# Kernel tuning notes

Hardware: AMD Instinct MI355X
Metric: run time of the kernel (lower is better)

The kernel has to match this reference:

```python
import jax, jax.numpy as jnp
import numpy as np

DIM = 768; DEPTH = 12; D_STATE = 64; D_CONV = 4; EXPAND = 2; HEADDIM = 64
VOCAB = 2048; MAXSEQ = 4096; B = 4; L = 2048
D_INNER = EXPAND * DIM            # 1536
NHEADS = D_INNER // HEADDIM       # 24
NG = 1                            # ngroups (Mamba2 default)
CONV_DIM = D_INNER + 2 * NG * D_STATE
D_IN_PROJ = 2 * D_INNER + 2 * NG * D_STATE + NHEADS
EPS = 1e-5


def silu(x):
    return x * jax.nn.sigmoid(x)


def layernorm(x, w, b):
    m = jnp.mean(x, -1, keepdims=True)
    v = jnp.mean((x - m) ** 2, -1, keepdims=True)
    return (x - m) * jax.lax.rsqrt(v + EPS) * w + b


def mamba2(x, in_w, cw, cb, dtb, a_log, dh, nw, ow):
    # x: (b, l, DIM)
    b, l, _ = x.shape
    zxbcdt = x @ in_w.T  # (b, l, D_IN_PROJ)
    z, xBC, dt = jnp.split(zxbcdt, [D_INNER, D_INNER + CONV_DIM], axis=-1)
    # causal depthwise conv1d over time
    xBC_p = jnp.pad(xBC, ((0, 0), (D_CONV - 1, 0), (0, 0))).transpose(0, 2, 1)  # (b, c, l+pad)
    conv = jax.lax.conv_general_dilated(
        xBC_p, cw[:, None, :], (1,), 'VALID',
        feature_group_count=CONV_DIM, dimension_numbers=('NCH', 'OIH', 'NCH'))
    xBC = silu(conv.transpose(0, 2, 1) + cb)  # (b, l, CONV_DIM)
    xs, Bm, Cm = jnp.split(xBC, [D_INNER, D_INNER + NG * D_STATE], axis=-1)
    xs = xs.reshape(b, l, NHEADS, HEADDIM)                # (b,l,h,p)
    dt = jax.nn.softplus(dt + dtb)                        # (b,l,h)
    A = -jnp.exp(a_log)                                   # (h,)
    dA = jnp.exp(dt * A)                                  # (b,l,h) decay per step

    def step(h, inp):
        # h: (b,h,p,n) SSM state
        dA_t, dt_t, x_t, B_t, C_t = inp
        dBx = jnp.einsum('bh,bhp,bn->bhpn', dt_t, x_t, B_t)
        h = h * dA_t[..., None, None] + dBx
        y = jnp.einsum('bhpn,bn->bhp', h, C_t)
        return h, y

    h0 = jnp.zeros((b, NHEADS, HEADDIM, D_STATE), x.dtype)
    xsT = (dA.transpose(1, 0, 2), dt.transpose(1, 0, 2), xs.transpose(1, 0, 2, 3),
           Bm.transpose(1, 0, 2), Cm.transpose(1, 0, 2))
    _, ys = jax.lax.scan(step, h0, xsT)                   # (l,b,h,p)
    y = ys.transpose(1, 0, 2, 3) + dh[None, None, :, None] * xs
    y = y.reshape(b, l, D_INNER)
    # gated RMSNorm (norm of y*silu(z)), then output projection
    y = y * silu(z)
    y = y * jax.lax.rsqrt(jnp.mean(y * y, -1, keepdims=True) + EPS) * nw
    return y @ ow.T


def setup_inputs() -> dict:
    key = jax.random.key(0)
    ks = jax.random.split(key, 12)
    init = lambda k, shape, s=0.02: (jax.random.normal(k, shape) * s).astype(jnp.float32)
    inp = {
        'token_emb': init(ks[0], (VOCAB, DIM)),
        'pos_emb': init(ks[1], (MAXSEQ, DIM)),
        'ln_w': jnp.ones((DEPTH, DIM), jnp.float32),
        'ln_b': jnp.zeros((DEPTH, DIM), jnp.float32),
        'in_proj_w': init(ks[2], (DEPTH, D_IN_PROJ, DIM)),
        'conv_w': init(ks[3], (DEPTH, CONV_DIM, D_CONV), 0.2),
        'conv_b': jnp.zeros((DEPTH, CONV_DIM), jnp.float32),
        'dt_bias': init(ks[4], (DEPTH, NHEADS), 0.5),
        'A_log': jnp.log(jax.random.uniform(ks[5], (DEPTH, NHEADS), minval=1.0, maxval=16.0)).astype(jnp.float32),
        'D_param': jnp.ones((DEPTH, NHEADS), jnp.float32),
        'norm_w': jnp.ones((DEPTH, D_INNER), jnp.float32),
        'out_proj_w': init(ks[6], (DEPTH, DIM, D_INNER)),
        'normf_w': jnp.ones((DIM,), jnp.float32),
        'normf_b': jnp.zeros((DIM,), jnp.float32),
        'head_w': init(ks[7], (VOCAB, DIM)),
        'input_ids': jax.random.randint(ks[8], (B, L), 0, VOCAB),
        'labels': jax.random.randint(ks[9], (B, L), 0, VOCAB),
    }
    return inp


def reference(token_emb, pos_emb, ln_w, ln_b, in_proj_w, conv_w, conv_b, dt_bias,
              A_log, D_param, norm_w, out_proj_w, normf_w, normf_b, head_w,
              input_ids, labels):
    b, n = input_ids.shape
    positions = jnp.arange(n) % MAXSEQ
    x = token_emb[input_ids] + pos_emb[positions][None]   # (b, n, DIM)

    def layer_fn(xc, p):
        lw, lb, iw, cw, cb, dtb, alog, dh, nw, ow = p
        return xc + mamba2(layernorm(xc, lw, lb), iw, cw, cb, dtb, alog, dh, nw, ow), None

    x, _ = jax.lax.scan(layer_fn, x,
                        (ln_w, ln_b, in_proj_w, conv_w, conv_b, dt_bias,
                         A_log, D_param, norm_w, out_proj_w))
    x = layernorm(x, normf_w, normf_b)
    logits = x @ head_w.T                                  # (b, n, VOCAB)
    sl = logits[:, :-1, :].reshape(-1, VOCAB)
    tl = labels[:, 1:].reshape(-1)
    logp = jax.nn.log_softmax(sl, -1)
    loss = -jnp.take_along_axis(logp, tl[:, None], axis=1).mean()
    return loss, logits
```

## Files before the change

### kernel.cpp

```cpp
#include <hip/hip_runtime.h>
#include <hip/hip_bf16.h>
#include <stdint.h>

#define DIMM   768
#define NLAYER 12
#define DST    64
#define DINNER 1536
#define NH     24
#define CONVD  1664
#define DINP   3224
#define NB     4
#define LL     2048
#define ROWS   (NB*LL)
#define VOC    2048
#define Q      128
#define NCH    (LL/Q)

typedef float f32x4 __attribute__((ext_vector_type(4)));
typedef short s16x8 __attribute__((ext_vector_type(8)));

#define MFMA(acc, a, b) asm volatile("v_mfma_f32_16x16x32_bf16 %0, %1, %2, %0" : "+v"(acc) : "v"(a), "v"(b))
#define FENCE4(v) asm volatile("s_nop 7" : "+v"(v))
#define GLL16(g, l) __builtin_amdgcn_global_load_lds( \
    (const __attribute__((address_space(1))) uint32_t*)(g), \
    (__attribute__((address_space(3))) uint32_t*)(l), 16, 0, 0)

__device__ __forceinline__ unsigned short f2bf(float f) {
  unsigned int u = __float_as_uint(f);
  u = (u + 0x7fffu + ((u >> 16) & 1u)) >> 16;
  return (unsigned short)u;
}
__device__ __forceinline__ float bf2f(unsigned short u) {
  return __uint_as_float(((unsigned int)u) << 16);
}
__device__ __forceinline__ float softplus_f(float v) {
  return (v > 20.f) ? v : log1pf(__expf(v));
}

__device__ __forceinline__ uint4 pack8(float4 a, float4 b) {
  union { unsigned short us[8]; uint4 q; } pk;
  pk.us[0] = f2bf(a.x); pk.us[1] = f2bf(a.y); pk.us[2] = f2bf(a.z); pk.us[3] = f2bf(a.w);
  pk.us[4] = f2bf(b.x); pk.us[5] = f2bf(b.y); pk.us[6] = f2bf(b.z); pk.us[7] = f2bf(b.w);
  return pk.q;
}

__device__ __forceinline__ float blk_sum(float v, float* red, int tid) {
  #pragma unroll
  for (int o = 32; o > 0; o >>= 1) v += __shfl_down(v, o, 64);
  __syncthreads();
  if ((tid & 63) == 0) red[tid >> 6] = v;
  __syncthreads();
  return red[0] + red[1] + red[2] + red[3];
}

__device__ __forceinline__ float blk_max(float v, float* red, int tid) {
  #pragma unroll
  for (int o = 32; o > 0; o >>= 1) v = fmaxf(v, __shfl_down(v, o, 64));
  __syncthreads();
  if ((tid & 63) == 0) red[tid >> 6] = v;
  __syncthreads();
  return fmaxf(fmaxf(red[0], red[1]), fmaxf(red[2], red[3]));
}

__global__ __launch_bounds__(256) void cvt_kernel(
    const float* __restrict__ s, unsigned short* __restrict__ d, int n8)
{
  int i = blockIdx.x * 256 + threadIdx.x;
  if (i < n8) {
    float4 a = ((const float4*)s)[i*2];
    float4 b = ((const float4*)s)[i*2 + 1];
    ((uint4*)d)[i] = pack8(a, b);
  }
}

__global__ __launch_bounds__(256) void cvtlayer_kernel(
    const float* __restrict__ ip, const float* __restrict__ op,
    const float* __restrict__ nw, unsigned short* __restrict__ ipb,
    unsigned short* __restrict__ opb)
{
  const int ipn8 = DINP*DIMM/8;
  const int opn8 = DIMM*DINNER/8;
  int i = blockIdx.x * 256 + threadIdx.x;
  if (i < ipn8) {
    float4 a = ((const float4*)ip)[i*2];
    float4 b = ((const float4*)ip)[i*2 + 1];
    ((uint4*)ipb)[i] = pack8(a, b);
  } else if (i < ipn8 + opn8) {
    int j = i - ipn8;
    int k = (j*8) % DINNER;
    float4 a = ((const float4*)op)[j*2];
    float4 b = ((const float4*)op)[j*2 + 1];
    float4 na = *(const float4*)(nw + k);
    float4 nb = *(const float4*)(nw + k + 4);
    a.x *= na.x; a.y *= na.y; a.z *= na.z; a.w *= na.w;
    b.x *= nb.x; b.y *= nb.y; b.z *= nb.z; b.w *= nb.w;
    ((uint4*)opb)[j] = pack8(a, b);
  }
}

__global__ __launch_bounds__(256) void embed_kernel(
    const float* __restrict__ tok, const float* __restrict__ pos,
    const int* __restrict__ ids, float* __restrict__ X)
{
  int idx = blockIdx.x * 256 + threadIdx.x;
  int row = idx / DIMM, d = idx % DIMM;
  int l = row & (LL - 1);
  X[idx] = tok[(size_t)ids[row] * DIMM + d] + pos[(size_t)l * DIMM + d];
}

__global__ __launch_bounds__(256) void ln_kernel(
    const float* __restrict__ X, const float* __restrict__ w,
    const float* __restrict__ b, unsigned short* __restrict__ Ob)
{
  __shared__ float red[8];
  int row = blockIdx.x, tid = threadIdx.x;
  const float* x = X + (size_t)row * DIMM;
  float v0 = x[tid], v1 = x[tid + 256], v2 = x[tid + 512];
  float mean = blk_sum(v0 + v1 + v2, red, tid) * (1.f / 768.f);
  float d0 = v0 - mean, d1 = v1 - mean, d2 = v2 - mean;
  float var = blk_sum(d0*d0 + d1*d1 + d2*d2, red, tid) * (1.f / 768.f);
  float rs = rsqrtf(var + 1e-5f);
  unsigned short* ob = Ob + (size_t)row * DIMM;
  ob[tid]       = f2bf(d0 * rs * w[tid]       + b[tid]);
  ob[tid + 256] = f2bf(d1 * rs * w[tid + 256] + b[tid + 256]);
  ob[tid + 512] = f2bf(d2 * rs * w[tid + 512] + b[tid + 512]);
}

template<int OUTM>
__global__ __launch_bounds__(256) void gemm_kernel(
    const unsigned short* __restrict__ A, const unsigned short* __restrict__ W,
    void* __restrict__ Cp, const float* __restrict__ RS,
    int Nreal, int K, int lda, int ldw, int ldc)
{
  __shared__ unsigned short As[128*32];
  __shared__ unsigned short Bs[128*32];
  const int tid = threadIdx.x;
  const int wave = tid >> 6, lane = tid & 63;
  const int wr = wave >> 1, wc = wave & 1;
  const int l15 = lane & 15, l4 = lane >> 4;
  const int bm = blockIdx.x * 128, bn = blockIdx.y * 128;
  f32x4 acc[4][4] = {};

  const int srow = lane >> 2;
  const int scol = (lane & 3) * 8;
  const unsigned short* aptr[2];
  const unsigned short* wptr[2];
  unsigned short* alds[2];
  unsigned short* blds[2];
  #pragma unroll
  for (int j = 0; j < 2; j++) {
    int row = (wave*2 + j)*16 + srow;
    aptr[j] = A + (size_t)(bm + row) * lda + scol;
    int wrow = bn + row; if (wrow > Nreal - 1) wrow = Nreal - 1;
    wptr[j] = W + (size_t)wrow * ldw + scol;
    alds[j] = &As[(wave*2 + j) * 512];
    blds[j] = &Bs[(wave*2 + j) * 512];
  }

  for (int k0 = 0; k0 < K; k0 += 32) {
    __syncthreads();
    #pragma unroll
    for (int j = 0; j < 2; j++) {
      GLL16(aptr[j], alds[j]);
      GLL16(wptr[j], blds[j]);
      aptr[j] += 32; wptr[j] += 32;
    }
    __syncthreads();
    s16x8 af[4], bfr[4];
    #pragma unroll
    for (int mi = 0; mi < 4; mi++)
      af[mi] = *(const s16x8*)&As[(wr*64 + mi*16 + l15)*32 + l4*8];
    #pragma unroll
    for (int ni = 0; ni < 4; ni++)
      bfr[ni] = *(const s16x8*)&Bs[(wc*64 + ni*16 + l15)*32 + l4*8];
    #pragma unroll
    for (int mi = 0; mi < 4; mi++)
      #pragma unroll
      for (int ni = 0; ni < 4; ni++)
        MFMA(acc[mi][ni], af[mi], bfr[ni]);
  }
  #pragma unroll
  for (int mi = 0; mi < 4; mi++)
    #pragma unroll
    for (int ni = 0; ni < 4; ni++)
      FENCE4(acc[mi][ni]);
  const int row0 = bm + wr*64 + l4*4;
  const int colb = bn + wc*64 + l15;
  #pragma unroll
  for (int mi = 0; mi < 4; mi++) {
    #pragma unroll
    for (int ni = 0; ni < 4; ni++) {
      int col = colb + ni*16;
      if (col < Nreal) {
        #pragma unroll
        for (int r = 0; r < 4; r++) {
          int rowm = row0 + mi*16 + r;
          size_t idx = (size_t)rowm * ldc + col;
          if (OUTM == 0)      ((float*)Cp)[idx] = acc[mi][ni][r];
          else if (OUTM == 1) ((float*)Cp)[idx] += RS[rowm] * acc[mi][ni][r];
          else                ((unsigned short*)Cp)[idx] = f2bf(acc[mi][ni][r]);
        }
      }
    }
  }
}

__global__ __launch_bounds__(256) void conv_kernel(
    const unsigned short* __restrict__ ZX, const float* __restrict__ cw,
    const float* __restrict__ cb, unsigned short* __restrict__ XC)
{
  int idx = blockIdx.x * 256 + threadIdx.x;
  int c8 = idx % 208, row = idx / 208;
  int c = c8 * 8;
  int l = row & (LL - 1);
  const unsigned short* z = ZX + (size_t)row * DINP + DINNER + c;
  s16x8 x0 = *(const s16x8*)z;
  s16x8 x1 = {}, x2 = {}, x3 = {};
  bool h1 = l >= 1, h2 = l >= 2, h3 = l >= 3;
  if (h1) x1 = *(const s16x8*)(z - DINP);
  if (h2) x2 = *(const s16x8*)(z - 2*DINP);
  if (h3) x3 = *(const s16x8*)(z - 3*DINP);
  union { unsigned short us[8]; uint4 q; } o;
  #pragma unroll
  for (int j = 0; j < 8; j++) {
    float4 w = ((const float4*)cw)[c + j];
    float a = cb[c + j] + bf2f((unsigned short)x0[j]) * w.w;
    if (h1) a += bf2f((unsigned short)x1[j]) * w.z;
    if (h2) a += bf2f((unsigned short)x2[j]) * w.y;
    if (h3) a += bf2f((unsigned short)x3[j]) * w.x;
    o.us[j] = f2bf(a / (1.f + __expf(-a)));
  }
  *(uint4*)(XC + (size_t)row * CONVD + c) = o.q;
}

__global__ __launch_bounds__(256) void chunkstate_kernel(
    const unsigned short* __restrict__ XC_, const unsigned short* __restrict__ ZX_,
    const float* __restrict__ dtbp, const float* __restrict__ alogp,
    float* __restrict__ HC_)
{
  __shared__ unsigned short XT[64*136];
  __shared__ unsigned short BT[64*136];
  __shared__ float cum_sh[Q], wgt_sh[Q];
  __shared__ float carry;
  const int tid = threadIdx.x;
  const int b = blockIdx.x >> 4, c = blockIdx.x & 15, h = blockIdx.y;
  const size_t row0 = (size_t)b*LL + c*Q;

  const float dtbv = dtbp[h];
  const float nA = -__expf(alogp[h]);
  float v = 0.f, dtv = 0.f;
  if (tid < Q) {
    float vraw = bf2f(ZX_[(row0 + tid)*DINP + 3200 + h]) + dtbv;
    dtv = softplus_f(vraw);
    v = dtv * nA;
    #pragma unroll
    for (int off = 1; off < 64; off <<= 1) {
      float u = __shfl_up(v, off, 64);
      if ((tid & 63) >= off) v += u;
    }
  }
  if (tid == 63) carry = v;
  __syncthreads();
  if (tid >= 64 && tid < Q) v += carry;
  if (tid < Q) cum_sh[tid] = v;
  __syncthreads();
  if (tid < Q) wgt_sh[tid] = __expf(cum_sh[Q-1] - v) * dtv;
  __syncthreads();

  const int p  = tid & 63;
  const int s0 = (tid >> 6) * 2;
  const unsigned short* xb = XC_ + row0 * CONVD;
  #pragma unroll
  for (int i = 0; i < 16; i++) {
    int s = s0 + i*8;
    float x0 = bf2f(xb[(size_t)s*CONVD     + h*64 + p]) * wgt_sh[s];
    float x1 = bf2f(xb[(size_t)(s+1)*CONVD + h*64 + p]) * wgt_sh[s+1];
    *(unsigned int*)&XT[p*136 + s] = (unsigned int)f2bf(x0) | ((unsigned int)f2bf(x1) << 16);
    unsigned int bb = (unsigned int)xb[(size_t)s*CONVD + DINNER + p]
                    | ((unsigned int)xb[(size_t)(s+1)*CONVD + DINNER + p] << 16);
    *(unsigned int*)&BT[p*136 + s] = bb;
  }
  __syncthreads();

  const int wave = tid >> 6, lane = tid & 63, l15 = lane & 15, l4 = lane >> 4;
  const int wr = wave >> 1, wc = wave & 1;
  f32x4 acc[2][2] = {};
  #pragma unroll
  for (int ks = 0; ks < 4; ks++) {
    int kof = ks*32 + l4*8;
    s16x8 a0 = *(const s16x8*)&XT[(wr*32      + l15)*136 + kof];
    s16x8 a1 = *(const s16x8*)&XT[(wr*32 + 16 + l15)*136 + kof];
    s16x8 b0 = *(const s16x8*)&BT[(wc*32      + l15)*136 + kof];
    s16x8 b1 = *(const s16x8*)&BT[(wc*32 + 16 + l15)*136 + kof];
    MFMA(acc[0][0], a0, b0); MFMA(acc[0][1], a0, b1);
    MFMA(acc[1][0], a1, b0); MFMA(acc[1][1], a1, b1);
  }
  #pragma unroll
  for (int mi = 0; mi < 2; mi++)
    #pragma unroll
    for (int ni = 0; ni < 2; ni++)
      FENCE4(acc[mi][ni]);
  size_t base = (((size_t)(b*NH + h))*NCH + c)*4096;
  #pragma unroll
  for (int mi = 0; mi < 2; mi++)
    #pragma unroll
    for (int ni = 0; ni < 2; ni++)
      #pragma unroll
      for (int r = 0; r < 4; r++)
        HC_[base + (size_t)(wr*32 + mi*16 + l4*4 + r)*64 + wc*32 + ni*16 + l15] = acc[mi][ni][r];
}

__global__ __launch_bounds__(256) void scan2_kernel(
    const float* __restrict__ HC_, float* __restrict__ HIN_,
    const unsigned short* __restrict__ ZX_, const float* __restrict__ dtbp,
    const float* __restrict__ alogp)
{
  __shared__ float dec[NCH];
  int bh = blockIdx.x, b = bh / NH, h = bh % NH;
  int q = blockIdx.y;
  int t = threadIdx.x;
  const float dtbv = dtbp[h];
  const float nA = -__expf(alogp[h]);
  float part = 0.f;
  #pragma unroll
  for (int i = 0; i < 8; i++) {
    float vraw = bf2f(ZX_[((size_t)b*LL + t*8 + i)*DINP + 3200 + h]) + dtbv;
    part += softplus_f(vraw) * nA;
  }
  #pragma unroll
  for (int off = 1; off < 16; off <<= 1) part += __shfl_xor(part, off, 16);
  if ((t & 15) == 0) dec[t >> 4] = __expf(part);
  __syncthreads();
  float st[4] = {0.f, 0.f, 0.f, 0.f};
  for (int c = 0; c < NCH; c++) {
    float d = dec[c];
    size_t base = ((size_t)bh*NCH + c)*4096 + q*1024;
    #pragma unroll
    for (int i = 0; i < 4; i++) {
      int idx = i*256 + t;
      HIN_[base + idx] = st[i];
      st[i] = st[i]*d + HC_[base + idx];
    }
  }
}

__global__ __launch_bounds__(256) void ydec_kernel(
    const unsigned short* __restrict__ XC_, const unsigned short* __restrict__ ZX_,
    const float* __restrict__ dtbp, const float* __restrict__ alogp,
    const float* __restrict__ HIN_, const float* __restrict__ Dp_,
    unsigned short* __restrict__ Y_)
{
  __shared__ unsigned short POOL[128*72*2];
  __shared__ unsigned short Hs[64*72];
  __shared__ unsigned short XTs[64*136];
  __shared__ float cum_sh[Q], dt_sh[Q];
  __shared__ float carry;
  unsigned short* Cs = POOL;
  unsigned short* Bs = POOL + 128*72;
  unsigned short* Ms = POOL;

  const int tid = threadIdx.x;
  const int b = blockIdx.x >> 4, c = blockIdx.x & 15, h = blockIdx.y;
  const size_t row0 = (size_t)b*LL + c*Q;

  const float dtbv = dtbp[h];
  const float nA = -__expf(alogp[h]);
  float v = 0.f, dtv = 0.f;
  if (tid < Q) {
    float vraw = bf2f(ZX_[(row0 + tid)*DINP + 3200 + h]) + dtbv;
    dtv = softplus_f(vraw);
    v = dtv * nA;
    #pragma unroll
    for (int off = 1; off < 64; off <<= 1) {
      float u = __shfl_up(v, off, 64);
      if ((tid & 63) >= off) v += u;
    }
  }
  if (tid == 63) carry = v;
  __syncthreads();
  if (tid >= 64 && tid < Q) v += carry;
  if (tid < Q) { cum_sh[tid] = v; dt_sh[tid] = dtv; }

  const int p  = tid & 63;
  const int s0 = (tid >> 6) * 2;
  const unsigned short* xb = XC_ + row0 * CONVD;
  #pragma unroll
  for (int i = 0; i < 16; i++) {
    int s = s0 + i*8;
    Cs[(size_t)s*72 + p]     = xb[(size_t)s*CONVD     + DINNER + DST + p];
    Cs[(size_t)(s+1)*72 + p] = xb[(size_t)(s+1)*CONVD + DINNER + DST + p];
    Bs[(size_t)s*72 + p]     = xb[(size_t)s*CONVD     + DINNER + p];
    Bs[(size_t)(s+1)*72 + p] = xb[(size_t)(s+1)*CONVD + DINNER + p];
    unsigned int xx = (unsigned int)xb[(size_t)s*CONVD + h*64 + p]
                    | ((unsigned int)xb[(size_t)(s+1)*CONVD + h*64 + p] << 16);
    *(unsigned int*)&XTs[p*136 + s] = xx;
  }
  {
    size_t hb = (((size_t)(b*NH + h))*NCH + c)*4096;
    #pragma unroll
    for (int i = 0; i < 16; i++) {
      int idx = i*256 + tid;
      Hs[(idx >> 6)*72 + (idx & 63)] = f2bf(HIN_[hb + idx]);
    }
  }
  __syncthreads();

  const int wv = tid >> 6, lane = tid & 63, l15 = lane & 15, l4 = lane >> 4;
  const int tb = wv * 32;

  f32x4 g[2][8] = {};
  f32x4 yacc[2][4] = {};
  #pragma unroll
  for (int ks = 0; ks < 2; ks++) {
    int kof = ks*32 + l4*8;
    s16x8 a0 = *(const s16x8*)&Cs[(size_t)(tb      + l15)*72 + kof];
    s16x8 a1 = *(const s16x8*)&Cs[(size_t)(tb + 16 + l15)*72 + kof];
    #pragma unroll
    for (int ni = 0; ni < 8; ni++) {
      if (ni <= 2*wv + 1) {
        s16x8 bfr = *(const s16x8*)&Bs[(size_t)(ni*16 + l15)*72 + kof];
        if (ni <= 2*wv) MFMA(g[0][ni], a0, bfr);
        MFMA(g[1][ni], a1, bfr);
      }
    }
    #pragma unroll
    for (int ni2 = 0; ni2 < 4; ni2++) {
      s16x8 hf = *(const s16x8*)&Hs[(size_t)(ni2*16 + l15)*72 + kof];
      MFMA(yacc[0][ni2], a0, hf);
      MFMA(yacc[1][ni2], a1, hf);
    }
  }
  __syncthreads();

  #pragma unroll
  for (int mi = 0; mi < 2; mi++) {
    #pragma unroll
    for (int ni = 0; ni < 8; ni++) {
      FENCE4(g[mi][ni]);
      int t0 = tb + mi*16 + l4*4;
      int s  = ni*16 + l15;
      float ds = dt_sh[s], cs = cum_sh[s];
      #pragma unroll
      for (int r = 0; r < 4; r++) {
        int tt = t0 + r;
        float val = (s <= tt) ? g[mi][ni][r] * __expf(cum_sh[tt] - cs) * ds : 0.f;
        Ms[(size_t)tt*136 + s] = f2bf(val);
      }
    }
  }

  float er[2][4];
  #pragma unroll
  for (int mi = 0; mi < 2; mi++)
    #pragma unroll
    for (int r = 0; r < 4; r++)
      er[mi][r] = __expf(cum_sh[tb + mi*16 + l4*4 + r]);
  #pragma unroll
  for (int mi = 0; mi < 2; mi++)
    #pragma unroll
    for (int ni2 = 0; ni2 < 4; ni2++) {
      FENCE4(yacc[mi][ni2]);
      #pragma unroll
      for (int r = 0; r < 4; r++) yacc[mi][ni2][r] *= er[mi][r];
      FENCE4(yacc[mi][ni2]);
    }

  #pragma unroll
  for (int ks = 0; ks < 4; ks++) {
    int kof = ks*32 + l4*8;
    s16x8 a0 = *(const s16x8*)&Ms[(size_t)(tb      + l15)*136 + kof];
    s16x8 a1 = *(const s16x8*)&Ms[(size_t)(tb + 16 + l15)*136 + kof];
    #pragma unroll
    for (int ni2 = 0; ni2 < 4; ni2++) {
      s16x8 xf = *(const s16x8*)&XTs[(size_t)(ni2*16 + l15)*136 + kof];
      MFMA(yacc[0][ni2], a0, xf);
      MFMA(yacc[1][ni2], a1, xf);
    }
  }
  #pragma unroll
  for (int mi = 0; mi < 2; mi++)
    #pragma unroll
    for (int ni2 = 0; ni2 < 4; ni2++)
      FENCE4(yacc[mi][ni2]);

  float Dv = Dp_[h];
  #pragma unroll
  for (int mi = 0; mi < 2; mi++) {
    #pragma unroll
    for (int ni2 = 0; ni2 < 4; ni2++) {
      #pragma unroll
      for (int r = 0; r < 4; r++) {
        int t = tb + mi*16 + l4*4 + r;
        int pc = ni2*16 + l15;
        float xv = bf2f(XTs[pc*136 + t]);
        float yv = yacc[mi][ni2][r] + Dv * xv;
        size_t row = row0 + t;
        float zv = bf2f(ZX_[row*DINP + h*64 + pc]);
        Y_[row*DINNER + h*64 + pc] = f2bf(yv * (zv / (1.f + __expf(-zv))));
      }
    }
  }
}

__global__ __launch_bounds__(256) void rs_kernel(
    const unsigned short* __restrict__ Y, float* __restrict__ RS)
{
  __shared__ float red[8];
  int row = blockIdx.x, tid = threadIdx.x;
  const unsigned short* y = Y + (size_t)row * DINNER;
  float sq = 0.f;
  if (tid < 192) {
    s16x8 u = *(const s16x8*)&y[tid*8];
    #pragma unroll
    for (int i = 0; i < 8; i++) { float f = bf2f((unsigned short)u[i]); sq += f*f; }
  }
  float ms = blk_sum(sq, red, tid) * (1.f / 1536.f);
  if (tid == 0) RS[row] = rsqrtf(ms + 1e-5f);
}

__global__ void zero_kernel(float* __restrict__ a) { a[0] = 0.f; }

__global__ __launch_bounds__(256) void loss_kernel(
    const float* __restrict__ logits, const int* __restrict__ labels,
    float* __restrict__ acc)
{
  __shared__ float red[8];
  int i = blockIdx.x;
  int b = i / (LL - 1), l = i % (LL - 1);
  const float* lr = logits + ((size_t)b * LL + l) * VOC;
  int tid = threadIdx.x;
  float4 v0 = ((const float4*)lr)[tid*2];
  float4 v1 = ((const float4*)lr)[tid*2 + 1];
  float mx = fmaxf(fmaxf(fmaxf(v0.x, v0.y), fmaxf(v0.z, v0.w)),
                   fmaxf(fmaxf(v1.x, v1.y), fmaxf(v1.z, v1.w)));
  mx = blk_max(mx, red, tid);
  float se = __expf(v0.x - mx) + __expf(v0.y - mx) + __expf(v0.z - mx) + __expf(v0.w - mx)
           + __expf(v1.x - mx) + __expf(v1.y - mx) + __expf(v1.z - mx) + __expf(v1.w - mx);
  se = blk_sum(se, red, tid);
  if (tid == 0) {
    int lab = labels[b * LL + l + 1];
    float lp = lr[lab] - mx - __logf(se);
    atomicAdd(acc, -lp);
  }
}

__global__ void fin_kernel(float* __restrict__ out, const float* __restrict__ acc) {
  out[0] = acc[0] * (1.f / 8188.f);
}

extern "C" void kernel_launch(void* const* d_in, const int* in_sizes, int n_in,
                              void* d_out, int out_size, void* d_ws, size_t ws_size,
                              hipStream_t stream)
{
  const float* tok  = (const float*)d_in[0];
  const float* pos  = (const float*)d_in[1];
  const float* lnw  = (const float*)d_in[2];
  const float* lnb  = (const float*)d_in[3];
  const float* ipw  = (const float*)d_in[4];
  const float* cw   = (const float*)d_in[5];
  const float* cb   = (const float*)d_in[6];
  const float* dtb  = (const float*)d_in[7];
  const float* alog = (const float*)d_in[8];
  const float* dpar = (const float*)d_in[9];
  const float* nw   = (const float*)d_in[10];
  const float* opw  = (const float*)d_in[11];
  const float* nfw  = (const float*)d_in[12];
  const float* nfb  = (const float*)d_in[13];
  const float* hw   = (const float*)d_in[14];
  const int*   ids  = (const int*)d_in[15];
  const int*   labs = (const int*)d_in[16];
  float* out = (float*)d_out;

  char* ws = (char*)d_ws;
  float*          X    = (float*)(ws);
  unsigned short* ZX   = (unsigned short*)(ws +  25165824ull);
  unsigned short* XC   = (unsigned short*)(ws +  77987840ull);
  unsigned short* Ybf  = (unsigned short*)(ws + 105250816ull);
  unsigned short* XNb  = (unsigned short*)(ws + 130416640ull);
  unsigned short* IPWb = (unsigned short*)(ws + 142999552ull);
  unsigned short* OPWb = (unsigned short*)(ws + 147951616ull);
  unsigned short* HWb  = (unsigned short*)(ws + 150310912ull);
  float*          HC   = (float*)(ws + 153456640ull);
  float*          RS   = (float*)(ws + 178622464ull);
  float*          ACC  = (float*)(ws + 178655232ull);
  float*          HIN  = out + 1 + 8388608;

  embed_kernel<<<ROWS*DIMM/256, 256, 0, stream>>>(tok, pos, ids, X);
  cvt_kernel<<<(VOC*DIMM/8 + 255)/256, 256, 0, stream>>>(hw, HWb, VOC*DIMM/8);

  const int cvtg = (DINP*DIMM/8 + DIMM*DINNER/8 + 255)/256;
  for (int l = 0; l < NLAYER; l++) {
    cvtlayer_kernel<<<cvtg, 256, 0, stream>>>(
        ipw + (size_t)l*DINP*DIMM, opw + (size_t)l*DIMM*DINNER,
        nw + (size_t)l*DINNER, IPWb, OPWb);

    ln_kernel<<<ROWS, 256, 0, stream>>>(X, lnw + l*DIMM, lnb + l*DIMM, XNb);

    dim3 g1(64, 26);
    gemm_kernel<2><<<g1, 256, 0, stream>>>(XNb, IPWb, ZX, nullptr,
                                           DINP, DIMM, DIMM, DIMM, DINP);

    conv_kernel<<<ROWS*208/256, 256, 0, stream>>>(ZX, cw + l*CONVD*4, cb + l*CONVD, XC);

    dim3 gs(NB*NCH, NH);
    chunkstate_kernel<<<gs, 256, 0, stream>>>(XC, ZX, dtb + l*NH, alog + l*NH, HC);
    dim3 g2s(NB*NH, 4);
    scan2_kernel<<<g2s, 256, 0, stream>>>(HC, HIN, ZX, dtb + l*NH, alog + l*NH);
    ydec_kernel<<<gs, 256, 0, stream>>>(XC, ZX, dtb + l*NH, alog + l*NH, HIN,
                                        dpar + l*NH, Ybf);

    rs_kernel<<<ROWS, 256, 0, stream>>>(Ybf, RS);

    dim3 g2(64, 6);
    gemm_kernel<1><<<g2, 256, 0, stream>>>(Ybf, OPWb, X, RS,
                                           DIMM, DINNER, DINNER, DINNER, DIMM);
  }

  ln_kernel<<<ROWS, 256, 0, stream>>>(X, nfw, nfb, XNb);
  dim3 g3(64, 16);
  gemm_kernel<0><<<g3, 256, 0, stream>>>(XNb, HWb, out + 1, nullptr,
                                         VOC, DIMM, DIMM, DIMM, VOC);

  zero_kernel<<<1, 1, 0, stream>>>(ACC);
  loss_kernel<<<NB*(LL-1), 256, 0, stream>>>(out + 1, labs, ACC);
  fin_kernel<<<1, 1, 0, stream>>>(out, ACC);
}
```

Measured before the change: 3.105 ms.

## Batch weight conversion, fuse RMS norm into ydec, cache dt cumsums, wave-per-row loss

All layer weights are now converted to bf16 in a single launch up front instead of once per layer. The sum-of-squares for the gated RMSNorm is accumulated in ydec via atomics, which removes rs_kernel. The chunkstate kernel stores the per-step dt cumsums and chunk decays so that scan2 and ydec no longer recompute softplus and prefix sums. The loss kernel uses one wave per row. The trade-offs are extra workspace, atomic float adds with nondeterministic summation order, and scratch buffers placed inside the output region.

```diff
diff --git a/kernel.cpp b/kernel.cpp
--- a/kernel.cpp
+++ b/kernel.cpp
@@ -53,48 +53,35 @@
   return red[0] + red[1] + red[2] + red[3];
 }
 
-__device__ __forceinline__ float blk_max(float v, float* red, int tid) {
-  #pragma unroll
-  for (int o = 32; o > 0; o >>= 1) v = fmaxf(v, __shfl_down(v, o, 64));
-  __syncthreads();
-  if ((tid & 63) == 0) red[tid >> 6] = v;
-  __syncthreads();
-  return fmaxf(fmaxf(red[0], red[1]), fmaxf(red[2], red[3]));
-}
-
-__global__ __launch_bounds__(256) void cvt_kernel(
-    const float* __restrict__ s, unsigned short* __restrict__ d, int n8)
-{
+__global__ __launch_bounds__(256) void cvtall_kernel(
+    const float* __restrict__ ipw, const float* __restrict__ opw,
+    const float* __restrict__ nw, const float* __restrict__ hw,
+    unsigned short* __restrict__ ipb, unsigned short* __restrict__ opb,
+    unsigned short* __restrict__ hwb)
+{
+  const int IPN8 = NLAYER*DINP*DIMM/8;
+  const int OPN8 = NLAYER*DIMM*DINNER/8;
+  const int HWN8 = VOC*DIMM/8;
   int i = blockIdx.x * 256 + threadIdx.x;
-  if (i < n8) {
-    float4 a = ((const float4*)s)[i*2];
-    float4 b = ((const float4*)s)[i*2 + 1];
-    ((uint4*)d)[i] = pack8(a, b);
-  }
-}
-
-__global__ __launch_bounds__(256) void cvtlayer_kernel(
-    const float* __restrict__ ip, const float* __restrict__ op,
-    const float* __restrict__ nw, unsigned short* __restrict__ ipb,
-    unsigned short* __restrict__ opb)
-{
-  const int ipn8 = DINP*DIMM/8;
-  const int opn8 = DIMM*DINNER/8;
-  int i = blockIdx.x * 256 + threadIdx.x;
-  if (i < ipn8) {
-    float4 a = ((const float4*)ip)[i*2];
-    float4 b = ((const float4*)ip)[i*2 + 1];
+  if (i < IPN8) {
+    float4 a = ((const float4*)ipw)[i*2];
+    float4 b = ((const float4*)ipw)[i*2 + 1];
     ((uint4*)ipb)[i] = pack8(a, b);
-  } else if (i < ipn8 + opn8) {
-    int j = i - ipn8;
+  } else if (i < IPN8 + OPN8) {
+    int j = i - IPN8;
+    int layer = j / (DIMM*DINNER/8);
     int k = (j*8) % DINNER;
-    float4 a = ((const float4*)op)[j*2];
-    float4 b = ((const float4*)op)[j*2 + 1];
-    float4 na = *(const float4*)(nw + k);
-    float4 nb = *(const float4*)(nw + k + 4);
+    const float* nwl = nw + layer*DINNER;
+    float4 a = ((const float4*)opw)[j*2];
+    float4 b = ((const float4*)opw)[j*2 + 1];
+    float4 na = *(const float4*)(nwl + k);
+    float4 nb = *(const float4*)(nwl + k + 4);
     a.x *= na.x; a.y *= na.y; a.z *= na.z; a.w *= na.w;
     b.x *= nb.x; b.y *= nb.y; b.z *= nb.z; b.w *= nb.w;
     ((uint4*)opb)[j] = pack8(a, b);
+  } else if (i < IPN8 + OPN8 + HWN8) {
+    int j = i - IPN8 - OPN8;
+    ((uint4*)hwb)[j] = pack8(((const float4*)hw)[j*2], ((const float4*)hw)[j*2 + 1]);
   }
 }
 
@@ -197,7 +184,10 @@
           int rowm = row0 + mi*16 + r;
           size_t idx = (size_t)rowm * ldc + col;
           if (OUTM == 0)      ((float*)Cp)[idx] = acc[mi][ni][r];
-          else if (OUTM == 1) ((float*)Cp)[idx] += RS[rowm] * acc[mi][ni][r];
+          else if (OUTM == 1) {
+            float rsv = rsqrtf(RS[rowm] * (1.f/1536.f) + 1e-5f);
+            ((float*)Cp)[idx] += rsv * acc[mi][ni][r];
+          }
           else                ((unsigned short*)Cp)[idx] = f2bf(acc[mi][ni][r]);
         }
       }
@@ -207,9 +197,11 @@
 
 __global__ __launch_bounds__(256) void conv_kernel(
     const unsigned short* __restrict__ ZX, const float* __restrict__ cw,
-    const float* __restrict__ cb, unsigned short* __restrict__ XC)
+    const float* __restrict__ cb, unsigned short* __restrict__ XC,
+    float* __restrict__ RS)
 {
   int idx = blockIdx.x * 256 + threadIdx.x;
+  if (idx < ROWS) RS[idx] = 0.f;
   int c8 = idx % 208, row = idx / 208;
   int c = c8 * 8;
   int l = row & (LL - 1);
@@ -236,7 +228,7 @@
 __global__ __launch_bounds__(256) void chunkstate_kernel(
     const unsigned short* __restrict__ XC_, const unsigned short* __restrict__ ZX_,
     const float* __restrict__ dtbp, const float* __restrict__ alogp,
-    float* __restrict__ HC_)
+    float* __restrict__ HC_, float2* __restrict__ DTC_, float* __restrict__ CDEC_)
 {
   __shared__ unsigned short XT[64*136];
   __shared__ unsigned short BT[64*136];
@@ -245,6 +237,7 @@
   const int tid = threadIdx.x;
   const int b = blockIdx.x >> 4, c = blockIdx.x & 15, h = blockIdx.y;
   const size_t row0 = (size_t)b*LL + c*Q;
+  const size_t bhc = (size_t)(b*NH + h)*NCH + c;
 
   const float dtbv = dtbp[h];
   const float nA = -__expf(alogp[h]);
@@ -264,7 +257,12 @@
   if (tid >= 64 && tid < Q) v += carry;
   if (tid < Q) cum_sh[tid] = v;
   __syncthreads();
-  if (tid < Q) wgt_sh[tid] = __expf(cum_sh[Q-1] - v) * dtv;
+  if (tid < Q) {
+    wgt_sh[tid] = __expf(cum_sh[Q-1] - v) * dtv;
+    float2 cd; cd.x = v; cd.y = dtv;
+    DTC_[bhc*Q + tid] = cd;
+  }
+  if (tid == Q-1) CDEC_[bhc] = __expf(v);
   __syncthreads();
 
   const int p  = tid & 63;
@@ -300,7 +298,7 @@
     #pragma unroll
     for (int ni = 0; ni < 2; ni++)
       FENCE4(acc[mi][ni]);
-  size_t base = (((size_t)(b*NH + h))*NCH + c)*4096;
+  size_t base = bhc*4096;
   #pragma unroll
   for (int mi = 0; mi < 2; mi++)
     #pragma unroll
@@ -312,24 +310,13 @@
 
 __global__ __launch_bounds__(256) void scan2_kernel(
     const float* __restrict__ HC_, float* __restrict__ HIN_,
-    const unsigned short* __restrict__ ZX_, const float* __restrict__ dtbp,
-    const float* __restrict__ alogp)
+    const float* __restrict__ CDEC_)
 {
   __shared__ float dec[NCH];
-  int bh = blockIdx.x, b = bh / NH, h = bh % NH;
+  int bh = blockIdx.x;
   int q = blockIdx.y;
   int t = threadIdx.x;
-  const float dtbv = dtbp[h];
-  const float nA = -__expf(alogp[h]);
-  float part = 0.f;
-  #pragma unroll
-  for (int i = 0; i < 8; i++) {
-    float vraw = bf2f(ZX_[((size_t)b*LL + t*8 + i)*DINP + 3200 + h]) + dtbv;
-    part += softplus_f(vraw) * nA;
-  }
-  #pragma unroll
-  for (int off = 1; off < 16; off <<= 1) part += __shfl_xor(part, off, 16);
-  if ((t & 15) == 0) dec[t >> 4] = __expf(part);
+  if (t < NCH) dec[t] = CDEC_[bh*NCH + t];
   __syncthreads();
   float st[4] = {0.f, 0.f, 0.f, 0.f};
   for (int c = 0; c < NCH; c++) {
@@ -346,15 +333,14 @@
 
 __global__ __launch_bounds__(256) void ydec_kernel(
     const unsigned short* __restrict__ XC_, const unsigned short* __restrict__ ZX_,
-    const float* __restrict__ dtbp, const float* __restrict__ alogp,
-    const float* __restrict__ HIN_, const float* __restrict__ Dp_,
-    unsigned short* __restrict__ Y_)
+    const float2* __restrict__ DTC_, const float* __restrict__ HIN_,
+    const float* __restrict__ Dp_, unsigned short* __restrict__ Y_,
+    float* __restrict__ RS_)
 {
   __shared__ unsigned short POOL[128*72*2];
   __shared__ unsigned short Hs[64*72];
   __shared__ unsigned short XTs[64*136];
   __shared__ float cum_sh[Q], dt_sh[Q];
-  __shared__ float carry;
   unsigned short* Cs = POOL;
   unsigned short* Bs = POOL + 128*72;
   unsigned short* Ms = POOL;
@@ -362,24 +348,12 @@
   const int tid = threadIdx.x;
   const int b = blockIdx.x >> 4, c = blockIdx.x & 15, h = blockIdx.y;
   const size_t row0 = (size_t)b*LL + c*Q;
-
-  const float dtbv = dtbp[h];
-  const float nA = -__expf(alogp[h]);
-  float v = 0.f, dtv = 0.f;
+  const size_t bhc = (size_t)(b*NH + h)*NCH + c;
+
   if (tid < Q) {
-    float vraw = bf2f(ZX_[(row0 + tid)*DINP + 3200 + h]) + dtbv;
-    dtv = softplus_f(vraw);
-    v = dtv * nA;
-    #pragma unroll
-    for (int off = 1; off < 64; off <<= 1) {
-      float u = __shfl_up(v, off, 64);
-      if ((tid & 63) >= off) v += u;
-    }
-  }
-  if (tid == 63) carry = v;
-  __syncthreads();
-  if (tid >= 64 && tid < Q) v += carry;
-  if (tid < Q) { cum_sh[tid] = v; dt_sh[tid] = dtv; }
+    float2 cd = DTC_[bhc*Q + tid];
+    cum_sh[tid] = cd.x; dt_sh[tid] = cd.y;
+  }
 
   const int p  = tid & 63;
   const int s0 = (tid >> 6) * 2;
@@ -396,7 +370,7 @@
     *(unsigned int*)&XTs[p*136 + s] = xx;
   }
   {
-    size_t hb = (((size_t)(b*NH + h))*NCH + c)*4096;
+    size_t hb = bhc*4096;
     #pragma unroll
     for (int i = 0; i < 16; i++) {
       int idx = i*256 + tid;
@@ -484,6 +458,7 @@
       FENCE4(yacc[mi][ni2]);
 
   float Dv = Dp_[h];
+  float sq[2][4] = {};
   #pragma unroll
   for (int mi = 0; mi < 2; mi++) {
     #pragma unroll
@@ -496,26 +471,23 @@
         float yv = yacc[mi][ni2][r] + Dv * xv;
         size_t row = row0 + t;
         float zv = bf2f(ZX_[row*DINP + h*64 + pc]);
-        Y_[row*DINNER + h*64 + pc] = f2bf(yv * (zv / (1.f + __expf(-zv))));
+        float yg = yv * (zv / (1.f + __expf(-zv)));
+        Y_[row*DINNER + h*64 + pc] = f2bf(yg);
+        sq[mi][r] += yg * yg;
       }
     }
   }
-}
-
-__global__ __launch_bounds__(256) void rs_kernel(
-    const unsigned short* __restrict__ Y, float* __restrict__ RS)
-{
-  __shared__ float red[8];
-  int row = blockIdx.x, tid = threadIdx.x;
-  const unsigned short* y = Y + (size_t)row * DINNER;
-  float sq = 0.f;
-  if (tid < 192) {
-    s16x8 u = *(const s16x8*)&y[tid*8];
-    #pragma unroll
-    for (int i = 0; i < 8; i++) { float f = bf2f((unsigned short)u[i]); sq += f*f; }
-  }
-  float ms = blk_sum(sq, red, tid) * (1.f / 1536.f);
-  if (tid == 0) RS[row] = rsqrtf(ms + 1e-5f);
+  #pragma unroll
+  for (int mi = 0; mi < 2; mi++) {
+    #pragma unroll
+    for (int r = 0; r < 4; r++) {
+      float vsum = sq[mi][r];
+      #pragma unroll
+      for (int off = 1; off < 16; off <<= 1) vsum += __shfl_xor(vsum, off, 64);
+      if (l15 == 0)
+        atomicAdd(&RS_[row0 + tb + mi*16 + l4*4 + r], vsum);
+    }
+  }
 }
 
 __global__ void zero_kernel(float* __restrict__ a) { a[0] = 0.f; }
@@ -524,24 +496,35 @@
     const float* __restrict__ logits, const int* __restrict__ labels,
     float* __restrict__ acc)
 {
-  __shared__ float red[8];
-  int i = blockIdx.x;
+  __shared__ float red[4];
+  int wv = threadIdx.x >> 6, lane = threadIdx.x & 63;
+  int i = blockIdx.x * 4 + wv;
   int b = i / (LL - 1), l = i % (LL - 1);
   const float* lr = logits + ((size_t)b * LL + l) * VOC;
-  int tid = threadIdx.x;
-  float4 v0 = ((const float4*)lr)[tid*2];
-  float4 v1 = ((const float4*)lr)[tid*2 + 1];
-  float mx = fmaxf(fmaxf(fmaxf(v0.x, v0.y), fmaxf(v0.z, v0.w)),
-                   fmaxf(fmaxf(v1.x, v1.y), fmaxf(v1.z, v1.w)));
-  mx = blk_max(mx, red, tid);
-  float se = __expf(v0.x - mx) + __expf(v0.y - mx) + __expf(v0.z - mx) + __expf(v0.w - mx)
-           + __expf(v1.x - mx) + __expf(v1.y - mx) + __expf(v1.z - mx) + __expf(v1.w - mx);
-  se = blk_sum(se, red, tid);
-  if (tid == 0) {
+  const float4* lr4 = (const float4*)lr;
+  float4 v[8];
+  #pragma unroll
+  for (int j = 0; j < 8; j++) v[j] = lr4[j*64 + lane];
+  float mx = -1e30f;
+  #pragma unroll
+  for (int j = 0; j < 8; j++)
+    mx = fmaxf(mx, fmaxf(fmaxf(v[j].x, v[j].y), fmaxf(v[j].z, v[j].w)));
+  #pragma unroll
+  for (int o = 32; o > 0; o >>= 1) mx = fmaxf(mx, __shfl_xor(mx, o, 64));
+  float se = 0.f;
+  #pragma unroll
+  for (int j = 0; j < 8; j++)
+    se += __expf(v[j].x - mx) + __expf(v[j].y - mx)
+        + __expf(v[j].z - mx) + __expf(v[j].w - mx);
+  #pragma unroll
+  for (int o = 32; o > 0; o >>= 1) se += __shfl_xor(se, o, 64);
+  if (lane == 0) {
     int lab = labels[b * LL + l + 1];
-    float lp = lr[lab] - mx - __logf(se);
-    atomicAdd(acc, -lp);
-  }
+    red[wv] = lr[lab] - mx - __logf(se);
+  }
+  __syncthreads();
+  if (threadIdx.x == 0)
+    atomicAdd(acc, -(red[0] + red[1] + red[2] + red[3]));
 }
 
 __global__ void fin_kernel(float* __restrict__ out, const float* __restrict__ acc) {
@@ -578,41 +561,38 @@
   unsigned short* Ybf  = (unsigned short*)(ws + 105250816ull);
   unsigned short* XNb  = (unsigned short*)(ws + 130416640ull);
   unsigned short* IPWb = (unsigned short*)(ws + 142999552ull);
-  unsigned short* OPWb = (unsigned short*)(ws + 147951616ull);
-  unsigned short* HWb  = (unsigned short*)(ws + 150310912ull);
-  float*          HC   = (float*)(ws + 153456640ull);
-  float*          RS   = (float*)(ws + 178622464ull);
-  float*          ACC  = (float*)(ws + 178655232ull);
-  float*          HIN  = out + 1 + 8388608;
+  unsigned short* OPWb = (unsigned short*)(ws + 202424320ull);
+  unsigned short* HWb  = (unsigned short*)(ws + 230735872ull);
+  float2*         DTC  = (float2*)(ws + 233881600ull);
+  float*          CDEC = (float*)(ws + 235454464ull);
+  float*          RS   = (float*)(ws + 235460608ull);
+  float*          ACC  = (float*)(ws + 235493376ull);
+  float*          HC   = out + 1;
+  float*          HIN  = out + 1 + 6291456;
 
   embed_kernel<<<ROWS*DIMM/256, 256, 0, stream>>>(tok, pos, ids, X);
-  cvt_kernel<<<(VOC*DIMM/8 + 255)/256, 256, 0, stream>>>(hw, HWb, VOC*DIMM/8);
-
-  const int cvtg = (DINP*DIMM/8 + DIMM*DINNER/8 + 255)/256;
+  {
+    const int tot = NLAYER*DINP*DIMM/8 + NLAYER*DIMM*DINNER/8 + VOC*DIMM/8;
+    cvtall_kernel<<<(tot + 255)/256, 256, 0, stream>>>(ipw, opw, nw, hw, IPWb, OPWb, HWb);
+  }
+
   for (int l = 0; l < NLAYER; l++) {
-    cvtlayer_kernel<<<cvtg, 256, 0, stream>>>(
-        ipw + (size_t)l*DINP*DIMM, opw + (size_t)l*DIMM*DINNER,
-        nw + (size_t)l*DINNER, IPWb, OPWb);
-
     ln_kernel<<<ROWS, 256, 0, stream>>>(X, lnw + l*DIMM, lnb + l*DIMM, XNb);
 
     dim3 g1(64, 26);
-    gemm_kernel<2><<<g1, 256, 0, stream>>>(XNb, IPWb, ZX, nullptr,
+    gemm_kernel<2><<<g1, 256, 0, stream>>>(XNb, IPWb + (size_t)l*DINP*DIMM, ZX, nullptr,
                                            DINP, DIMM, DIMM, DIMM, DINP);
 
-    conv_kernel<<<ROWS*208/256, 256, 0, stream>>>(ZX, cw + l*CONVD*4, cb + l*CONVD, XC);
+    conv_kernel<<<ROWS*208/256, 256, 0, stream>>>(ZX, cw + l*CONVD*4, cb + l*CONVD, XC, RS);
 
     dim3 gs(NB*NCH, NH);
-    chunkstate_kernel<<<gs, 256, 0, stream>>>(XC, ZX, dtb + l*NH, alog + l*NH, HC);
+    chunkstate_kernel<<<gs, 256, 0, stream>>>(XC, ZX, dtb + l*NH, alog + l*NH, HC, DTC, CDEC);
     dim3 g2s(NB*NH, 4);
-    scan2_kernel<<<g2s, 256, 0, stream>>>(HC, HIN, ZX, dtb + l*NH, alog + l*NH);
-    ydec_kernel<<<gs, 256, 0, stream>>>(XC, ZX, dtb + l*NH, alog + l*NH, HIN,
-                                        dpar + l*NH, Ybf);
-
-    rs_kernel<<<ROWS, 256, 0, stream>>>(Ybf, RS);
+    scan2_kernel<<<g2s, 256, 0, stream>>>(HC, HIN, CDEC);
+    ydec_kernel<<<gs, 256, 0, stream>>>(XC, ZX, DTC, HIN, dpar + l*NH, Ybf, RS);
 
     dim3 g2(64, 6);
-    gemm_kernel<1><<<g2, 256, 0, stream>>>(Ybf, OPWb, X, RS,
+    gemm_kernel<1><<<g2, 256, 0, stream>>>(Ybf, OPWb + (size_t)l*DIMM*DINNER, X, RS,
                                            DIMM, DINNER, DINNER, DINNER, DIMM);
   }
 
@@ -622,6 +602,6 @@
                                          VOC, DIMM, DIMM, DIMM, VOC);
 
   zero_kernel<<<1, 1, 0, stream>>>(ACC);
-  loss_kernel<<<NB*(LL-1), 256, 0, stream>>>(out + 1, labs, ACC);
+  loss_kernel<<<2047, 256, 0, stream>>>(out + 1, labs, ACC);
   fin_kernel<<<1, 1, 0, stream>>>(out, ACC);
 }
```

After: 3.082 ms. About the same (-0.8%).
